# Kernel tuning notes

Hardware: AMD Instinct MI355X
Metric: run time of the kernel (lower is better)

## Reference

```python
import jax, jax.numpy as jnp
import numpy as np

C = 128  # in_channels

def setup_inputs() -> dict:
    key = jax.random.key(0)
    k1, k2, k3, k4 = jax.random.split(key, 4)
    b, c, h, w = 4, C, 64, 64
    feature0 = jax.random.normal(k1, (b, c, h, w), dtype=jnp.float32)
    flow = jax.random.normal(k2, (b, 2, h, w), dtype=jnp.float32)
    # Linear weights stored torch-style as [out, in]; xavier-uniform-like scale
    lim = float(np.sqrt(6.0 / (c + c)))
    Wq = jax.random.uniform(k3, (c, c), minval=-lim, maxval=lim, dtype=jnp.float32)
    Wk = jax.random.uniform(k4, (c, c), minval=-lim, maxval=lim, dtype=jnp.float32)
    bq = jnp.zeros((c,), dtype=jnp.float32)
    bk = jnp.zeros((c,), dtype=jnp.float32)
    return {"feature0": feature0, "flow": flow, "Wq": Wq, "bq": bq, "Wk": Wk, "bk": bk}

def reference(feature0, flow, Wq, bq, Wk, bk):
    b, c, h, w = feature0.shape
    n = h * w
    # [b, n, c]
    x = feature0.reshape(b, c, n).transpose(0, 2, 1)
    query = x @ Wq.T + bq                     # q_proj(feature0)
    key = query @ Wk.T + bk                   # NOTE: k_proj applied to query (as in source)
    value = flow.reshape(b, flow.shape[1], n).transpose(0, 2, 1)  # [b, n, 2]
    scores = jnp.einsum('bnc,bmc->bnm', query, key) / jnp.sqrt(jnp.float32(c))
    prob = jax.nn.softmax(scores, axis=-1)    # [b, n, n]
    out = jnp.einsum('bnm,bmv->bnv', prob, value)  # [b, n, 2]
    return out.reshape(b, h, w, value.shape[-1]).transpose(0, 3, 1, 2)
```

## Files before the change

kernel.cpp:

```cpp
#include <hip/hip_runtime.h>
#include <hip/hip_bf16.h>

constexpr int CH = 128;
constexpr int NPOS = 4096;
constexpr int NB = 4;
constexpr int SPLITS = 8;

typedef __bf16 bf16x8 __attribute__((ext_vector_type(8)));
typedef float f32x2 __attribute__((ext_vector_type(2)));
typedef float f32x16 __attribute__((ext_vector_type(16)));

constexpr float CSC = 0.08838834764831845f * 1.4426950408889634f;


__device__ __forceinline__ void async_copy16(const void* g, void* l) {
  auto gp = (const __attribute__((address_space(1))) unsigned int*)((uintptr_t)g);
  auto lp = (__attribute__((address_space(3))) unsigned int*)((uintptr_t)l);
  __builtin_amdgcn_global_load_lds(gp, lp, 16, 0, 0);
}

#define PIPE_BARRIER(N)                                              \
  asm volatile("s_waitcnt vmcnt(" #N ") lgkmcnt(0)\n\ts_barrier" ::: "memory")

__global__ __launch_bounds__(128) void fuse_w_kernel(
    const float* __restrict__ Wq, const float* __restrict__ bq,
    const float* __restrict__ Wk, const float* __restrict__ bk,
    __bf16* __restrict__ Wqb, __bf16* __restrict__ Wqkb,
    float* __restrict__ bqk) {
  __shared__ float red[CH];
  const int o = blockIdx.x;
  const int i = threadIdx.x;
  float acc = 0.f;
#pragma unroll 8
  for (int m = 0; m < CH; m++) acc += Wk[o * CH + m] * Wq[m * CH + i];
  Wqkb[o * CH + i] = (__bf16)acc;
  Wqb[o * CH + i] = (__bf16)Wq[o * CH + i];
  red[i] = Wk[o * CH + i] * bq[i];
  __syncthreads();
  if (i == 0) {
    float s = 0.f;
    for (int m = 0; m < CH; m++) s += red[m];
    bqk[o] = s + bk[o];
  }
}

__global__ __launch_bounds__(256) void proj_kernel(
    const float* __restrict__ feature0, const __bf16* __restrict__ Wqb,
    const float* __restrict__ bq, const __bf16* __restrict__ Wqkb,
    const float* __restrict__ bqk, __bf16* __restrict__ Qf,
    __bf16* __restrict__ Kf) {
  const int bid = blockIdx.x;
  const int b = (bid >> 1) & 3;
  const int rest = (bid >> 3) * 2 + (bid & 1);
  const int u = rest >> 1, z = rest & 1;
  const int n = threadIdx.x >> 6;
  const int lane = threadIdx.x & 63;
  const int half = lane >> 5, l31 = lane & 31;
  const int pos = u * 32 + l31;

  bf16x8 A[8];
#pragma unroll
  for (int ks = 0; ks < 8; ks++) {
    float v[8];
#pragma unroll
    for (int j = 0; j < 8; j++)
      v[j] = feature0[(size_t)(b * CH + ks * 16 + half * 8 + j) * NPOS + pos];
#pragma unroll
    for (int j = 0; j < 8; j++) A[ks][j] = (__bf16)v[j];
  }

  const __bf16* W = z ? Wqkb : Wqb;
  const float* bias = z ? bqk : bq;
  __bf16* Out = z ? Kf : Qf;
  const float scale = z ? 1.0f : CSC;

  const int co = n * 32 + l31;
  const bf16x8* Bp = (const bf16x8*)(W + co * CH + half * 8);
  f32x16 c = {0.f, 0.f, 0.f, 0.f, 0.f, 0.f, 0.f, 0.f,
              0.f, 0.f, 0.f, 0.f, 0.f, 0.f, 0.f, 0.f};
#pragma unroll
  for (int ks = 0; ks < 8; ks++)
    c = __builtin_amdgcn_mfma_f32_32x32x16_bf16(A[ks], Bp[ks * 2], c, 0, 0, 0);
  const float bv = bias[co];
  const int kf = n * 2 + (l31 >> 4);
  const int lanebit = (l31 >> 3) & 1;
  const int j = l31 & 7;
#pragma unroll
  for (int r = 0; r < 16; r++) {
    int roff = (r & 3) + 8 * (r >> 2) + 4 * half;
    Out[((((size_t)(b * (NPOS / 32) + u)) * 8 + kf) * 64 +
         (roff + 32 * lanebit)) * 8 + j] = (__bf16)((c[r] + bv) * scale);
  }
}

__global__ __launch_bounds__(512, 2) void attn_kernel(
    const __bf16* __restrict__ Qf, const __bf16* __restrict__ Kf,
    const float* __restrict__ flow, float* __restrict__ part) {
  __shared__ __bf16 Klds[3][8 * 512];
  __shared__ float flds[2 * 512];
  __shared__ float red[256 * 3];

  const int bid = blockIdx.x;
  const int b = (bid >> 1) & 3;
  const int u = (bid >> 3) * 2 + (bid & 1);
  const int split = u >> 4;
  const int qg = u & 15;

  const int tid = threadIdx.x;
  const int wave = tid >> 6, lane = tid & 63;
  const int half = lane >> 5, l31 = lane & 31;
  const int kbase = split * (NPOS / SPLITS);
  constexpr int NT = NPOS / SPLITS / 32;

  {
    const float* fl0 = flow + (size_t)(b * 2 + 0) * NPOS + kbase;
    const float* fl1 = flow + (size_t)(b * 2 + 1) * NPOS + kbase;
    flds[tid] = fl0[tid];
    flds[512 + tid] = fl1[tid];
  }

  const int qt = qg * 8 + wave;
  bf16x8 qf[8];
  {
    const bf16x8* Qp =
        (const bf16x8*)Qf + ((size_t)(b * (NPOS / 32) + qt) * 8) * 64 + lane;
#pragma unroll
    for (int kf = 0; kf < 8; kf++) qf[kf] = Qp[kf * 64];
  }

  const __bf16* Ktb = Kf + ((size_t)(b * (NPOS / 32) + (kbase >> 5))) * 4096;

  auto issue = [&](int t, int buf) {
    const __bf16* g = Ktb + (size_t)t * 4096;
    async_copy16(g + wave * 512 + lane * 8,
                 &Klds[buf][wave * 512 + lane * 8]);
  };
  issue(0, 0);
  issue(1, 1);

  float ls[16];
  f32x2 av[16];
#pragma unroll
  for (int r = 0; r < 16; r++) {
    ls[r] = 0.f;
    av[r] = f32x2{0.f, 0.f};
  }

  int bcur = 0, bnext = 2;
  for (int t = 0; t < NT; t++) {
    PIPE_BARRIER(1);
    if (t + 2 < NT) issue(t + 2, bnext);

    const __bf16* kb = &Klds[bcur][0];
    f32x16 c = {0.f, 0.f, 0.f, 0.f, 0.f, 0.f, 0.f, 0.f,
                0.f, 0.f, 0.f, 0.f, 0.f, 0.f, 0.f, 0.f};
#pragma unroll
    for (int kf = 0; kf < 8; kf++) {
      bf16x8 bfrag = *(const bf16x8*)(kb + kf * 512 + lane * 8);
      c = __builtin_amdgcn_mfma_f32_32x32x16_bf16(qf[kf], bfrag, c, 0, 0, 0);
    }
    const f32x2 v01 = {flds[t * 32 + l31], flds[512 + t * 32 + l31]};
#pragma unroll
    for (int r = 0; r < 16; r++) {
      float p = __builtin_amdgcn_exp2f(c[r]);
      ls[r] += p;
      av[r] += f32x2{p, p} * v01;
    }
    bcur = (bcur == 2) ? 0 : bcur + 1;
    bnext = (bnext == 2) ? 0 : bnext + 1;
  }

#pragma unroll
  for (int r = 0; r < 16; r++) {
#pragma unroll
    for (int st = 1; st < 32; st <<= 1) {
      ls[r] += __shfl_xor(ls[r], st, 64);
      av[r][0] += __shfl_xor(av[r][0], st, 64);
      av[r][1] += __shfl_xor(av[r][1], st, 64);
    }
  }
  if (l31 == 0) {
#pragma unroll
    for (int r = 0; r < 16; r++) {
      int ql = wave * 32 + (r & 3) + 8 * (r >> 2) + 4 * half;
      red[ql * 3 + 0] = ls[r];
      red[ql * 3 + 1] = av[r][0];
      red[ql * 3 + 2] = av[r][1];
    }
  }
  __syncthreads();
  for (int idx = tid; idx < 256 * 3; idx += 512) {
    int plane = idx >> 8, ql = idx & 255;
    part[((size_t)(plane * SPLITS + split) * NB + b) * NPOS + qg * 256 + ql] =
        red[ql * 3 + plane];
  }
}

__global__ __launch_bounds__(256) void combine_kernel(
    const float* __restrict__ part, float* __restrict__ out) {
  int t = blockIdx.x * 256 + threadIdx.x;
  int b = t >> 12, q = t & (NPOS - 1);
  float l = 0.f, x = 0.f, y = 0.f;
#pragma unroll
  for (int s = 0; s < SPLITS; s++) {
    l += part[((size_t)(0 * SPLITS + s) * NB + b) * NPOS + q];
    x += part[((size_t)(1 * SPLITS + s) * NB + b) * NPOS + q];
    y += part[((size_t)(2 * SPLITS + s) * NB + b) * NPOS + q];
  }
  float inv = 1.0f / l;
  out[(size_t)(b * 2 + 0) * NPOS + q] = x * inv;
  out[(size_t)(b * 2 + 1) * NPOS + q] = y * inv;
}

extern "C" void kernel_launch(void* const* d_in, const int* in_sizes, int n_in,
                              void* d_out, int out_size, void* d_ws,
                              size_t ws_size, hipStream_t stream) {
  const float* feature0 = (const float*)d_in[0];
  const float* flow = (const float*)d_in[1];
  const float* Wq = (const float*)d_in[2];
  const float* bq = (const float*)d_in[3];
  const float* Wk = (const float*)d_in[4];
  const float* bk = (const float*)d_in[5];
  float* out = (float*)d_out;

  char* ws = (char*)d_ws;
  __bf16* Qf = (__bf16*)ws;
  __bf16* Kf = (__bf16*)(ws + (4 << 20));
  __bf16* Wqb = (__bf16*)(ws + (8 << 20));
  __bf16* Wqkb = (__bf16*)(ws + (8 << 20) + (32 << 10));
  float* bqk = (float*)(ws + (8 << 20) + (64 << 10));
  float* part = (float*)(ws + (8 << 20) + (128 << 10));

  fuse_w_kernel<<<dim3(CH), 128, 0, stream>>>(Wq, bq, Wk, bk, Wqb, Wqkb, bqk);
  proj_kernel<<<dim3(1024), 256, 0, stream>>>(feature0, Wqb, bq, Wqkb, bqk, Qf,
                                              Kf);
  attn_kernel<<<dim3(512), 512, 0, stream>>>(Qf, Kf, flow, part);
  combine_kernel<<<dim3(NB * NPOS / 256), 256, 0, stream>>>(part, out);
}
```

Baseline: 113.5 us.

## Process two query tiles per wave in attention to reuse K fragments

Halves the attention block to 4 waves, and each wave now computes two 32-row query tiles against the same K fragment read from LDS. This halves LDS reads of K per MFMA and the number of waves sharing each barrier. Each wave issues two async copies per tile, so the wait count becomes 2. The cost is roughly double the accumulator and Q registers per wave and fewer resident waves to hide exp2 and MFMA latency.

```diff
diff --git a/kernel.cpp b/kernel.cpp
--- a/kernel.cpp
+++ b/kernel.cpp
@@ -93,7 +93,7 @@
   }
 }
 
-__global__ __launch_bounds__(512, 2) void attn_kernel(
+__global__ __launch_bounds__(256, 2) void attn_kernel(
     const __bf16* __restrict__ Qf, const __bf16* __restrict__ Kf,
     const float* __restrict__ flow, float* __restrict__ part) {
   __shared__ __bf16 Klds[3][8 * 512];
@@ -116,55 +116,74 @@
     const float* fl0 = flow + (size_t)(b * 2 + 0) * NPOS + kbase;
     const float* fl1 = flow + (size_t)(b * 2 + 1) * NPOS + kbase;
     flds[tid] = fl0[tid];
+    flds[256 + tid] = fl0[256 + tid];
     flds[512 + tid] = fl1[tid];
-  }
-
-  const int qt = qg * 8 + wave;
-  bf16x8 qf[8];
+    flds[768 + tid] = fl1[256 + tid];
+  }
+
+  const int qt0 = qg * 8 + wave;
+  const int qt1 = qg * 8 + 4 + wave;
+  bf16x8 qf0[8], qf1[8];
   {
-    const bf16x8* Qp =
-        (const bf16x8*)Qf + ((size_t)(b * (NPOS / 32) + qt) * 8) * 64 + lane;
-#pragma unroll
-    for (int kf = 0; kf < 8; kf++) qf[kf] = Qp[kf * 64];
+    const bf16x8* Qp0 =
+        (const bf16x8*)Qf + ((size_t)(b * (NPOS / 32) + qt0) * 8) * 64 + lane;
+    const bf16x8* Qp1 =
+        (const bf16x8*)Qf + ((size_t)(b * (NPOS / 32) + qt1) * 8) * 64 + lane;
+#pragma unroll
+    for (int kf = 0; kf < 8; kf++) {
+      qf0[kf] = Qp0[kf * 64];
+      qf1[kf] = Qp1[kf * 64];
+    }
   }
 
   const __bf16* Ktb = Kf + ((size_t)(b * (NPOS / 32) + (kbase >> 5))) * 4096;
 
   auto issue = [&](int t, int buf) {
     const __bf16* g = Ktb + (size_t)t * 4096;
-    async_copy16(g + wave * 512 + lane * 8,
-                 &Klds[buf][wave * 512 + lane * 8]);
+#pragma unroll
+    for (int cc = 0; cc < 2; cc++) {
+      int chunk = wave * 2 + cc;
+      async_copy16(g + chunk * 512 + lane * 8,
+                   &Klds[buf][chunk * 512 + lane * 8]);
+    }
   };
   issue(0, 0);
   issue(1, 1);
 
-  float ls[16];
-  f32x2 av[16];
+  float ls0[16], ls1[16];
+  f32x2 av0[16], av1[16];
 #pragma unroll
   for (int r = 0; r < 16; r++) {
-    ls[r] = 0.f;
-    av[r] = f32x2{0.f, 0.f};
+    ls0[r] = 0.f;
+    ls1[r] = 0.f;
+    av0[r] = f32x2{0.f, 0.f};
+    av1[r] = f32x2{0.f, 0.f};
   }
 
   int bcur = 0, bnext = 2;
   for (int t = 0; t < NT; t++) {
-    PIPE_BARRIER(1);
+    PIPE_BARRIER(2);
     if (t + 2 < NT) issue(t + 2, bnext);
 
     const __bf16* kb = &Klds[bcur][0];
-    f32x16 c = {0.f, 0.f, 0.f, 0.f, 0.f, 0.f, 0.f, 0.f,
-                0.f, 0.f, 0.f, 0.f, 0.f, 0.f, 0.f, 0.f};
+    f32x16 c0 = {0.f, 0.f, 0.f, 0.f, 0.f, 0.f, 0.f, 0.f,
+                 0.f, 0.f, 0.f, 0.f, 0.f, 0.f, 0.f, 0.f};
+    f32x16 c1 = c0;
 #pragma unroll
     for (int kf = 0; kf < 8; kf++) {
       bf16x8 bfrag = *(const bf16x8*)(kb + kf * 512 + lane * 8);
-      c = __builtin_amdgcn_mfma_f32_32x32x16_bf16(qf[kf], bfrag, c, 0, 0, 0);
+      c0 = __builtin_amdgcn_mfma_f32_32x32x16_bf16(qf0[kf], bfrag, c0, 0, 0, 0);
+      c1 = __builtin_amdgcn_mfma_f32_32x32x16_bf16(qf1[kf], bfrag, c1, 0, 0, 0);
     }
     const f32x2 v01 = {flds[t * 32 + l31], flds[512 + t * 32 + l31]};
 #pragma unroll
     for (int r = 0; r < 16; r++) {
-      float p = __builtin_amdgcn_exp2f(c[r]);
-      ls[r] += p;
-      av[r] += f32x2{p, p} * v01;
+      float p0 = __builtin_amdgcn_exp2f(c0[r]);
+      float p1 = __builtin_amdgcn_exp2f(c1[r]);
+      ls0[r] += p0;
+      ls1[r] += p1;
+      av0[r] += f32x2{p0, p0} * v01;
+      av1[r] += f32x2{p1, p1} * v01;
     }
     bcur = (bcur == 2) ? 0 : bcur + 1;
     bnext = (bnext == 2) ? 0 : bnext + 1;
@@ -174,22 +193,30 @@
   for (int r = 0; r < 16; r++) {
 #pragma unroll
     for (int st = 1; st < 32; st <<= 1) {
-      ls[r] += __shfl_xor(ls[r], st, 64);
-      av[r][0] += __shfl_xor(av[r][0], st, 64);
-      av[r][1] += __shfl_xor(av[r][1], st, 64);
+      ls0[r] += __shfl_xor(ls0[r], st, 64);
+      ls1[r] += __shfl_xor(ls1[r], st, 64);
+      av0[r][0] += __shfl_xor(av0[r][0], st, 64);
+      av0[r][1] += __shfl_xor(av0[r][1], st, 64);
+      av1[r][0] += __shfl_xor(av1[r][0], st, 64);
+      av1[r][1] += __shfl_xor(av1[r][1], st, 64);
     }
   }
   if (l31 == 0) {
 #pragma unroll
     for (int r = 0; r < 16; r++) {
-      int ql = wave * 32 + (r & 3) + 8 * (r >> 2) + 4 * half;
-      red[ql * 3 + 0] = ls[r];
-      red[ql * 3 + 1] = av[r][0];
-      red[ql * 3 + 2] = av[r][1];
+      int roff = (r & 3) + 8 * (r >> 2) + 4 * half;
+      int ql0 = wave * 32 + roff;
+      int ql1 = 128 + wave * 32 + roff;
+      red[ql0 * 3 + 0] = ls0[r];
+      red[ql0 * 3 + 1] = av0[r][0];
+      red[ql0 * 3 + 2] = av0[r][1];
+      red[ql1 * 3 + 0] = ls1[r];
+      red[ql1 * 3 + 1] = av1[r][0];
+      red[ql1 * 3 + 2] = av1[r][1];
     }
   }
   __syncthreads();
-  for (int idx = tid; idx < 256 * 3; idx += 512) {
+  for (int idx = tid; idx < 256 * 3; idx += 256) {
     int plane = idx >> 8, ql = idx & 255;
     part[((size_t)(plane * SPLITS + split) * NB + b) * NPOS + qg * 256 + ql] =
         red[ql * 3 + plane];
@@ -234,6 +261,6 @@
   fuse_w_kernel<<<dim3(CH), 128, 0, stream>>>(Wq, bq, Wk, bk, Wqb, Wqkb, bqk);
   proj_kernel<<<dim3(1024), 256, 0, stream>>>(feature0, Wqb, bq, Wqkb, bqk, Qf,
                                               Kf);
-  attn_kernel<<<dim3(512), 512, 0, stream>>>(Qf, Kf, flow, part);
+  attn_kernel<<<dim3(512), 256, 0, stream>>>(Qf, Kf, flow, part);
   combine_kernel<<<dim3(NB * NPOS / 256), 256, 0, stream>>>(part, out);
 }
```

Measured after the change: 114.6 us. No clear change (+1.0%).
